# Performance work log

Hardware: AMD Instinct MI355X
Metric: run time of the kernel (lower is better)

The kernel has to match this reference:

```python
import jax, jax.numpy as jnp
import numpy as np

N_SV = 8192      # current-frame supervoxels (rows of mean_features / sv_prob)
M_SV = 8192      # surrounding-frame supervoxels
C_FEAT = 96
N_CLS = 20
EPSILON = 0.03   # OT entropic regularizer (forward default)


def setup_inputs() -> dict:
    key = jax.random.key(0)
    ks = jax.random.split(key, 8)
    # near-rigid poses: identity + small perturbation (keeps inverse well-conditioned)
    posses = jnp.eye(4, dtype=jnp.float32)[None] + 0.05 * jax.random.normal(ks[0], (2, 4, 4), jnp.float32)
    return {
        "sur_sv_feature": jax.random.normal(ks[1], (M_SV, C_FEAT), jnp.float32),
        "sur_sv_coords": jax.random.normal(ks[2], (M_SV, 3), jnp.float32),
        "sur_sv_gt": jax.random.randint(ks[3], (M_SV,), 0, N_CLS),
        "sv_prob": jax.random.normal(ks[4], (N_SV, N_CLS), jnp.float32),
        "mean_features": jax.random.normal(ks[5], (N_SV, C_FEAT), jnp.float32),
        "ori_coords": jax.random.normal(ks[6], (N_SV, 3), jnp.float32),
        "posses": posses,
        "sv_gt_idx": jax.random.randint(ks[7], (N_SV,), 0, N_SV),
        "lg": M_SV,
    }


def reference(sur_sv_feature, sur_sv_coords, sur_sv_gt, sv_prob, mean_features,
              ori_coords, posses, sv_gt_idx, lg):
    # --- alignment (rev=1 branch): transform surrounding coords into current frame ---
    diff = jnp.linalg.inv(posses[1]) @ posses[0]                      # [4,4]
    homo = jnp.concatenate([sur_sv_coords,
                            jnp.ones((sur_sv_coords.shape[0], 1), sur_sv_coords.dtype)], axis=1)
    al_sur = (homo @ diff.T)[:, :3]                                   # [M,3]

    # --- fused affinity construction: cosine + exp(-l2) kernel + support mask ---
    w1 = jnp.linalg.norm(mean_features, axis=1, keepdims=True)        # [N,1]
    w2 = jnp.linalg.norm(sur_sv_feature, axis=1, keepdims=True)      # [M,1]
    feat_dist = 1.0 - (mean_features @ sur_sv_feature.T) / jnp.clip(w1 * w2.T, 1e-8)  # [N,M]
    coords_dist = jnp.sum((ori_coords[:, None, :] - al_sur[None, :, :]) ** 2, -1) / (0.5 ** 2)  # [N,M]
    support = (coords_dist < 10.0 ** 2).astype(jnp.float32)
    dist_matric = 1.0 + feat_dist - jnp.exp(-0.5 * coords_dist)
    K = jnp.exp(-dist_matric / EPSILON) * support                     # [N,M]

    # --- Sinkhorn loop: original uses constant u1,u2 on the RHS, so a,b are
    # loop-invariant; a single evaluation reproduces all 10 iterations exactly ---
    N, M = K.shape
    u2 = jnp.full((N,), 1.0 / N, jnp.float32)
    u1 = jnp.full((M,), 1.0 / M, jnp.float32)
    b = u2 / (K @ u1 + 1e-16)                                         # [N]
    a = u1 / (K.T @ u2 + 1e-16)                                       # [M]

    simlarity = (a[:, None] * K.T) * b[None, :]                       # diag(a) @ K.T @ diag(b), [M,N]
    simlarity = simlarity[:lg]

    sv_prob_updated = jax.nn.softmax(sv_prob, axis=1)                 # [N,ncls]
    sm_index = jnp.argmax(simlarity, axis=1)                          # [lg] in [0,N)
    onehot = jax.nn.one_hot(sur_sv_gt, N_CLS, dtype=jnp.float32)      # [M,ncls]
    tmpx = jnp.argmax(onehot[:lg], axis=1)                            # [lg]
    conf = sv_prob_updated[sm_index, tmpx]                            # diag of gather
    tmp_hi = conf > 0.1
    tmp = jnp.where(jnp.any(tmp_hi), tmp_hi, conf > 0.0)              # fallback threshold

    # masked scatter: out-of-range index N drops the update (mode='drop')
    idx = jnp.where(tmp, sm_index, N)
    sv_prob_updated = sv_prob_updated.at[idx].set(onehot[:lg], mode="drop")
    trust = jnp.zeros((N,), bool).at[idx].set(True, mode="drop")      # fixed-shape unique(sm_index)
    pre = jnp.argmax(sv_prob_updated, axis=1)

    return trust, sv_prob_updated, pre, sm_index
```

## Files before the change

### kernel.cpp

```cpp
#include <hip/hip_runtime.h>
#include <math.h>

typedef __attribute__((ext_vector_type(8))) short short8;
typedef __attribute__((ext_vector_type(16))) float floatx16;

#define NSV 8192
#define MSV 8192
#define CF 96
#define NCLS 20

#define C48 48.08983469629878f
#define C96 96.17966939259756f
#define CEV -2.885390081777927f

#define OFF_A0    0u
#define OFF_A1    1572864u
#define OFF_A2    3145728u
#define OFF_B0    4718592u
#define OFF_B1    6291456u
#define OFF_B2    7864320u
#define OFF_RV4   9437184u
#define OFF_CV4   9568256u
#define OFF_PROW  9699328u
#define OFF_SMENC 11796480u
#define OFF_SMIDX 11862016u
#define OFF_WIN   11894784u
#define OFF_CONF  11927552u
#define OFF_FLAG  11960320u

#define O_TRUST 0
#define O_PROB  NSV
#define O_PRE   (O_PROB + NSV*NCLS)
#define O_SM    (O_PRE + NSV)

__device__ __forceinline__ unsigned short bfr(float x) {
  unsigned u = __float_as_uint(x);
  return (unsigned short)((u + 0x7FFFu + ((u >> 16) & 1u)) >> 16);
}
__device__ __forceinline__ float bff(unsigned short h) {
  return __uint_as_float(((unsigned)h) << 16);
}
__device__ __forceinline__ float fexp2(float x) {
  float r; asm("v_exp_f32 %0, %1" : "=v"(r) : "v"(x)); return r;
}

__global__ void k_prep(const float* __restrict__ surf, const float* __restrict__ surc,
                       const float* __restrict__ meanf, const float* __restrict__ ori,
                       const float* __restrict__ posses, char* __restrict__ wsb) {
  __shared__ float dsh[12];
  if (threadIdx.x == 0) {
    double m[4][8];
    for (int r = 0; r < 4; ++r)
      for (int c = 0; c < 4; ++c) { m[r][c] = (double)posses[16 + r*4 + c]; m[r][4+c] = (r == c) ? 1.0 : 0.0; }
    for (int col = 0; col < 4; ++col) {
      int piv = col; double best = fabs(m[col][col]);
      for (int r = col+1; r < 4; ++r) { double v = fabs(m[r][col]); if (v > best) { best = v; piv = r; } }
      if (piv != col) for (int c = 0; c < 8; ++c) { double tt = m[col][c]; m[col][c] = m[piv][c]; m[piv][c] = tt; }
      double pv = m[col][col];
      for (int c = 0; c < 8; ++c) m[col][c] /= pv;
      for (int r = 0; r < 4; ++r) if (r != col) {
        double f = m[r][col];
        for (int c = 0; c < 8; ++c) m[r][c] -= f * m[col][c];
      }
    }
    for (int r = 0; r < 3; ++r)
      for (int c = 0; c < 4; ++c) {
        double s = 0.0;
        for (int k = 0; k < 4; ++k) s += m[r][4+k] * (double)posses[k*4 + c];
        dsh[r*4 + c] = (float)s;
      }
  }
  __syncthreads();
  int j = blockIdx.x*256 + threadIdx.x;
  if (j >= NSV) return;
  float d[12];
  #pragma unroll
  for (int q = 0; q < 12; ++q) d[q] = dsh[q];
  float x = surc[j*3+0], y = surc[j*3+1], z = surc[j*3+2];
  float ax = ((x*d[0] + y*d[1]) + z*d[2]) + d[3];
  float ay = ((x*d[4] + y*d[5]) + z*d[6]) + d[7];
  float az = ((x*d[8] + y*d[9]) + z*d[10]) + d[11];
  const float4* f2 = (const float4*)(surf  + (size_t)j*CF);
  const float4* f1 = (const float4*)(meanf + (size_t)j*CF);
  float s2 = 0.f, s1 = 0.f;
  #pragma unroll
  for (int kq = 0; kq < 24; ++kq) {
    float4 v = f2[kq]; s2 += v.x*v.x; s2 += v.y*v.y; s2 += v.z*v.z; s2 += v.w*v.w;
  }
  #pragma unroll
  for (int kq = 0; kq < 24; ++kq) {
    float4 v = f1[kq]; s1 += v.x*v.x; s1 += v.y*v.y; s1 += v.z*v.z; s1 += v.w*v.w;
  }
  float4 cvv; cvv.x = 1.0f/sqrtf(s2); cvv.y = ax; cvv.z = ay; cvv.w = az;
  ((float4*)(wsb + OFF_CV4))[j] = cvv;
  float4 rvv; rvv.x = 1.0f/sqrtf(s1); rvv.y = ori[j*3+0]; rvv.z = ori[j*3+1]; rvv.w = ori[j*3+2];
  ((float4*)(wsb + OFF_RV4))[j] = rvv;
}

__global__ void k_split(const float* __restrict__ meanf, const float* __restrict__ surf,
                        char* __restrict__ wsb) {
  const int NT = NSV*CF/4;
  int idx = blockIdx.x*256 + threadIdx.x;
  if (idx >= 2*NT) return;
  int m = idx >= NT;
  int e4 = idx - (m ? NT : 0);
  int base4 = e4 * 4;
  int row = base4 / CF;
  int k0  = base4 - row*CF;
  const float* src = m ? surf : meanf;
  float scale;
  if (m) scale = ((const float4*)(wsb + OFF_CV4))[row].x;
  else   scale = ((const float4*)(wsb + OFF_RV4))[row].x * C48;
  unsigned short* d0 = (unsigned short*)(wsb + (m ? OFF_B0 : OFF_A0));
  unsigned short* d1 = (unsigned short*)(wsb + (m ? OFF_B1 : OFF_A1));
  unsigned short* d2 = (unsigned short*)(wsb + (m ? OFF_B2 : OFF_A2));
  float4 v = *(const float4*)(src + base4);
  float xs[4] = {v.x*scale, v.y*scale, v.z*scale, v.w*scale};
  unsigned short h0[4], h1[4], h2[4];
  #pragma unroll
  for (int c = 0; c < 4; ++c) {
    float x = xs[c];
    unsigned short a0 = bfr(x);  float r1 = x - bff(a0);
    unsigned short a1 = bfr(r1); float r2 = r1 - bff(a1);
    h0[c] = a0; h1[c] = a1; h2[c] = bfr(r2);
  }
  int g   = row >> 5;
  int l31 = row & 31;
  int kc  = k0 >> 4;
  int hi  = (k0 >> 3) & 1;
  int e8  = k0 & 7;
  int offu = ((g*6 + kc) << 9) + (((hi << 5) | l31) << 3) + e8;
  *(ushort4*)(d0 + offu) = make_ushort4(h0[0], h0[1], h0[2], h0[3]);
  *(ushort4*)(d1 + offu) = make_ushort4(h1[0], h1[1], h1[2], h1[3]);
  *(ushort4*)(d2 + offu) = make_ushort4(h2[0], h2[1], h2[2], h2[3]);
}

template<int PASS>
__global__ __launch_bounds__(256, 2)
void k_gemm(char* __restrict__ wsb) {
  const float4* RV  = (const float4*)(wsb + OFF_RV4);
  const float4* CVC = (const float4*)(wsb + OFF_CV4);
  float* PROW = (float*)(wsb + OFF_PROW);
  unsigned long long* SME = (unsigned long long*)(wsb + OFF_SMENC);

  __shared__ unsigned long long redbuf[2][128];

  int t = threadIdx.x, lane = t & 63, wid = t >> 6;
  int wr = wid >> 1, wc = wid & 1, l31 = lane & 31, hi = lane >> 5;
  int flat = blockIdx.y*64 + blockIdx.x;
  int xcd = flat & 7, q = flat >> 3;
  int xr = xcd >> 1, xc = xcd & 1;
  int bi = xr*16 + (q & 15), bj = xc*32 + (q >> 4);
  int I0 = bi*128, J0 = bj*128;

  const char* pA[3][2];
  const char* pB[3][2];
  {
    int gA = (I0 >> 5) + wr*2;
    int gB = (J0 >> 5) + wc*2;
    unsigned offs[3] = {OFF_A0, OFF_A1, OFF_A2};
    unsigned offsB[3] = {OFF_B0, OFF_B1, OFF_B2};
    #pragma unroll
    for (int s = 0; s < 3; ++s)
      #pragma unroll
      for (int ti = 0; ti < 2; ++ti) {
        pA[s][ti] = wsb + offs[s]  + (((gA + ti)*6) << 10) + lane*16;
        pB[s][ti] = wsb + offsB[s] + (((gB + ti)*6) << 10) + lane*16;
      }
  }

  floatx16 acc[2][2];
  #pragma unroll
  for (int ti = 0; ti < 2; ++ti)
    #pragma unroll
    for (int tj = 0; tj < 2; ++tj)
      #pragma unroll
      for (int e = 0; e < 16; ++e) acc[ti][tj][e] = 0.f;

  short8 fa[3][2], fb[3][2];
  #pragma unroll
  for (int s = 0; s < 3; ++s)
    #pragma unroll
    for (int ti = 0; ti < 2; ++ti) {
      fa[s][ti] = *(const short8*)(pA[s][ti]);
      fb[s][ti] = *(const short8*)(pB[s][ti]);
    }

  #pragma unroll
  for (int kc = 0; kc < 6; ++kc) {
    short8 na[3][2], nb[3][2];
    if (kc < 5) {
      #pragma unroll
      for (int s = 0; s < 3; ++s)
        #pragma unroll
        for (int ti = 0; ti < 2; ++ti) {
          na[s][ti] = *(const short8*)(pA[s][ti] + (kc+1)*1024);
          nb[s][ti] = *(const short8*)(pB[s][ti] + (kc+1)*1024);
        }
    }
    #pragma unroll
    for (int ti = 0; ti < 2; ++ti)
      #pragma unroll
      for (int tj = 0; tj < 2; ++tj) {
        acc[ti][tj] = __builtin_amdgcn_mfma_f32_32x32x16_bf16(fa[0][ti], fb[0][tj], acc[ti][tj], 0, 0, 0);
        acc[ti][tj] = __builtin_amdgcn_mfma_f32_32x32x16_bf16(fa[0][ti], fb[1][tj], acc[ti][tj], 0, 0, 0);
        acc[ti][tj] = __builtin_amdgcn_mfma_f32_32x32x16_bf16(fa[1][ti], fb[0][tj], acc[ti][tj], 0, 0, 0);
        acc[ti][tj] = __builtin_amdgcn_mfma_f32_32x32x16_bf16(fa[1][ti], fb[1][tj], acc[ti][tj], 0, 0, 0);
        acc[ti][tj] = __builtin_amdgcn_mfma_f32_32x32x16_bf16(fa[0][ti], fb[2][tj], acc[ti][tj], 0, 0, 0);
        acc[ti][tj] = __builtin_amdgcn_mfma_f32_32x32x16_bf16(fa[2][ti], fb[0][tj], acc[ti][tj], 0, 0, 0);
      }
    if (kc < 5) {
      #pragma unroll
      for (int s = 0; s < 3; ++s)
        #pragma unroll
        for (int ti = 0; ti < 2; ++ti) { fa[s][ti] = na[s][ti]; fb[s][ti] = nb[s][ti]; }
    }
  }

  float4 cv[2];
  #pragma unroll
  for (int tj = 0; tj < 2; ++tj) cv[tj] = CVC[J0 + wc*64 + tj*32 + l31];

  if (PASS == 1) {
    float* rowred = (float*)redbuf;
    #pragma unroll
    for (int ti = 0; ti < 2; ++ti) {
      #pragma unroll
      for (int r = 0; r < 16; ++r) {
        int lr = wr*64 + ti*32 + (r & 3) + 8*(r >> 2) + 4*hi;
        int row = I0 + lr;
        float4 rv = RV[row];
        float rowp = 0.f;
        #pragma unroll
        for (int tj = 0; tj < 2; ++tj) {
          float dotv = acc[ti][tj][r];
          float dx = rv.y - cv[tj].y, dy = rv.z - cv[tj].z, dz = rv.w - cv[tj].w;
          float s3 = fmaf(dz, dz, fmaf(dy, dy, dx*dx));
          float ev = fexp2(s3 * CEV);
          float kv = fexp2(fmaf(ev, C48, dotv - C96));
          kv = (s3 < 25.0f) ? kv : 0.0f;
          rowp += kv;
        }
        rowp += __shfl_xor(rowp, 1);
        rowp += __shfl_xor(rowp, 2);
        rowp += __shfl_xor(rowp, 4);
        rowp += __shfl_xor(rowp, 8);
        rowp += __shfl_xor(rowp, 16);
        if (l31 == 0) rowred[wc*128 + lr] = rowp;
      }
    }
    __syncthreads();
    if (t < 128) PROW[(size_t)(I0 + t)*64 + bj] = rowred[t] + rowred[128 + t];
  } else {
    unsigned long long benc[2] = {0ull, 0ull};
    #pragma unroll
    for (int ti = 0; ti < 2; ++ti) {
      #pragma unroll
      for (int r = 0; r < 16; ++r) {
        int lr = wr*64 + ti*32 + (r & 3) + 8*(r >> 2) + 4*hi;
        int row = I0 + lr;
        float4 rv = RV[row];
        unsigned rinv = 0xFFFFFFFFu - (unsigned)row;
        #pragma unroll
        for (int tj = 0; tj < 2; ++tj) {
          float dotv = acc[ti][tj][r];
          float dx = rv.y - cv[tj].y, dy = rv.z - cv[tj].z, dz = rv.w - cv[tj].w;
          float s3 = fmaf(dz, dz, fmaf(dy, dy, dx*dx));
          float ev = fexp2(s3 * CEV);
          float kv = fexp2(fmaf(ev, C48, dotv - C96));
          kv = (s3 < 25.0f) ? kv : 0.0f;
          float val = kv * rv.x;
          unsigned long long e = ((unsigned long long)__float_as_uint(val) << 32)
                               | (unsigned long long)rinv;
          benc[tj] = (e > benc[tj]) ? e : benc[tj];
        }
      }
    }
    #pragma unroll
    for (int tj = 0; tj < 2; ++tj) {
      unsigned long long o = __shfl_xor(benc[tj], 32);
      if (o > benc[tj]) benc[tj] = o;
      if (hi == 0) redbuf[wr][wc*64 + tj*32 + l31] = benc[tj];
    }
    __syncthreads();
    if (t < 128) {
      unsigned long long e0 = redbuf[0][t], e1 = redbuf[1][t];
      atomicMax(SME + (J0 + t), e0 > e1 ? e0 : e1);
    }
  }
}

__global__ void k_bvec(char* __restrict__ wsb) {
  int i = blockIdx.x*256 + threadIdx.x;
  if (i >= NSV) return;
  const float* p = (const float*)(wsb + OFF_PROW) + (size_t)i*64;
  float s = 0.f;
  #pragma unroll
  for (int q = 0; q < 64; ++q) s += p[q];
  float b = 0x1p-13f / (s * 0x1p-13f + 1e-16f);
  ((float*)(wsb + OFF_RV4))[(size_t)i*4] = b;
  ((int*)(wsb + OFF_WIN))[i] = -1;
  ((unsigned long long*)(wsb + OFF_SMENC))[i] = 0ull;
  if (i == 0) *((int*)(wsb + OFF_FLAG)) = 0;
}

__global__ void k_softmax(const float* __restrict__ svp, float* __restrict__ out) {
  int i = blockIdx.x*256 + threadIdx.x;
  if (i >= NSV) return;
  const float* x = svp + (size_t)i*NCLS;
  float mx = x[0];
  for (int c = 1; c < NCLS; ++c) mx = fmaxf(mx, x[c]);
  float e[NCLS]; float s = 0.f;
  for (int c = 0; c < NCLS; ++c) { e[c] = expf(x[c] - mx); s += e[c]; }
  float* p = out + O_PROB + (size_t)i*NCLS;
  for (int c = 0; c < NCLS; ++c) p[c] = e[c]/s;
}

__global__ void k_conf(const int* __restrict__ gt, char* __restrict__ wsb, float* __restrict__ out) {
  int j = blockIdx.x*256 + threadIdx.x;
  if (j >= MSV) return;
  unsigned long long enc = ((const unsigned long long*)(wsb + OFF_SMENC))[j];
  int sm = (int)(0xFFFFFFFFu - (unsigned)(enc & 0xFFFFFFFFull));
  ((int*)(wsb + OFF_SMIDX))[j] = sm;
  out[O_SM + j] = (float)sm;
  float c = out[O_PROB + (size_t)sm*NCLS + gt[j]];
  ((float*)(wsb + OFF_CONF))[j] = c;
  unsigned long long m = __ballot(c > 0.1f);
  if ((threadIdx.x & 63) == 0 && m) atomicOr((int*)(wsb + OFF_FLAG), 1);
}

__global__ void k_winner(char* __restrict__ wsb) {
  int j = blockIdx.x*256 + threadIdx.x;
  if (j >= MSV) return;
  float c = ((const float*)(wsb + OFF_CONF))[j];
  int f = *((const int*)(wsb + OFF_FLAG));
  bool tm = f ? (c > 0.1f) : (c > 0.0f);
  if (tm) atomicMax(((int*)(wsb + OFF_WIN)) + ((const int*)(wsb + OFF_SMIDX))[j], j);
}

__global__ void k_final(const int* __restrict__ gt, float* __restrict__ out, const char* __restrict__ wsb) {
  int i = blockIdx.x*256 + threadIdx.x;
  if (i >= NSV) return;
  int w = ((const int*)(wsb + OFF_WIN))[i];
  float* row = out + O_PROB + (size_t)i*NCLS;
  if (w >= 0) {
    int g = gt[w];
    for (int c = 0; c < NCLS; ++c) row[c] = (c == g) ? 1.f : 0.f;
  }
  out[O_TRUST + i] = (w >= 0) ? 1.f : 0.f;
  float mx = row[0]; int pi = 0;
  for (int c = 1; c < NCLS; ++c) { float v = row[c]; if (v > mx) { mx = v; pi = c; } }
  out[O_PRE + i] = (float)pi;
}

extern "C" void kernel_launch(void* const* d_in, const int* in_sizes, int n_in,
                              void* d_out, int out_size, void* d_ws, size_t ws_size,
                              hipStream_t stream) {
  const float* surf  = (const float*)d_in[0];
  const float* surc  = (const float*)d_in[1];
  const int*   gt    = (const int*)d_in[2];
  const float* svp   = (const float*)d_in[3];
  const float* meanf = (const float*)d_in[4];
  const float* ori   = (const float*)d_in[5];
  const float* poss  = (const float*)d_in[6];
  float* out = (float*)d_out;
  char* wsb = (char*)d_ws;

  k_prep<<<NSV/256, 256, 0, stream>>>(surf, surc, meanf, ori, poss, wsb);
  k_split<<<1536, 256, 0, stream>>>(meanf, surf, wsb);
  k_gemm<1><<<dim3(64, 64), 256, 0, stream>>>(wsb);
  k_bvec<<<NSV/256, 256, 0, stream>>>(wsb);
  k_gemm<2><<<dim3(64, 64), 256, 0, stream>>>(wsb);
  k_softmax<<<NSV/256, 256, 0, stream>>>(svp, out);
  k_conf<<<MSV/256, 256, 0, stream>>>(gt, wsb, out);
  k_winner<<<MSV/256, 256, 0, stream>>>(wsb);
  k_final<<<NSV/256, 256, 0, stream>>>(gt, out, wsb);
}
```

Before: 294.2 us.

## Stage GEMM operand tiles through LDS with direct global-to-LDS loads

Replaces per-wave direct global register loads of the bf16 split operands with cooperative global_load_lds staging of the block's A and B tiles into 72KB of shared memory, in two K-halves. Each wave then reads its fragments from LDS, so operand tiles shared by the waves of a block are fetched from global memory once rather than once per wave. In exchange the per-half loads are no longer overlapped with MFMA work, extra barriers are added, and the large LDS footprint may cut occupancy below the two blocks per CU that the launch bounds request.

```diff
diff --git a/kernel.cpp b/kernel.cpp
--- a/kernel.cpp
+++ b/kernel.cpp
@@ -143,6 +143,7 @@
   float* PROW = (float*)(wsb + OFF_PROW);
   unsigned long long* SME = (unsigned long long*)(wsb + OFF_SMENC);
 
+  __shared__ char lds[73728];
   __shared__ unsigned long long redbuf[2][128];
 
   int t = threadIdx.x, lane = t & 63, wid = t >> 6;
@@ -153,21 +154,27 @@
   int bi = xr*16 + (q & 15), bj = xc*32 + (q >> 4);
   int I0 = bi*128, J0 = bj*128;
 
-  const char* pA[3][2];
-  const char* pB[3][2];
-  {
-    int gA = (I0 >> 5) + wr*2;
-    int gB = (J0 >> 5) + wc*2;
-    unsigned offs[3] = {OFF_A0, OFF_A1, OFF_A2};
-    unsigned offsB[3] = {OFF_B0, OFF_B1, OFF_B2};
-    #pragma unroll
-    for (int s = 0; s < 3; ++s)
-      #pragma unroll
-      for (int ti = 0; ti < 2; ++ti) {
-        pA[s][ti] = wsb + offs[s]  + (((gA + ti)*6) << 10) + lane*16;
-        pB[s][ti] = wsb + offsB[s] + (((gB + ti)*6) << 10) + lane*16;
-      }
-  }
+  const unsigned offsA[3] = {OFF_A0, OFF_A1, OFF_A2};
+  const unsigned offsB[3] = {OFF_B0, OFF_B1, OFF_B2};
+
+  auto stage = [&](int h) {
+    #pragma unroll
+    for (int qq = 0; qq < 18; ++qq) {
+      int p = qq*4 + wid;
+      int side = (p >= 36) ? 1 : 0;
+      int r = p - side*36;
+      int s = r / 12;
+      int rem = r - s*12;
+      int gl = rem / 3;
+      int c = rem - gl*3;
+      unsigned base = side ? offsB[s] : offsA[s];
+      int g = ((side ? J0 : I0) >> 5) + gl;
+      const char* gp = wsb + base + (((unsigned)(g*6 + h*3 + c)) << 10) + lane*16;
+      char* lp = lds + p*1024 + lane*16;
+      __builtin_amdgcn_global_load_lds((const __attribute__((address_space(1))) void*)gp,
+                                       (__attribute__((address_space(3))) void*)lp, 16, 0, 0);
+    }
+  };
 
   floatx16 acc[2][2];
   #pragma unroll
@@ -177,45 +184,40 @@
       #pragma unroll
       for (int e = 0; e < 16; ++e) acc[ti][tj][e] = 0.f;
 
-  short8 fa[3][2], fb[3][2];
-  #pragma unroll
-  for (int s = 0; s < 3; ++s)
-    #pragma unroll
-    for (int ti = 0; ti < 2; ++ti) {
-      fa[s][ti] = *(const short8*)(pA[s][ti]);
-      fb[s][ti] = *(const short8*)(pB[s][ti]);
-    }
-
-  #pragma unroll
-  for (int kc = 0; kc < 6; ++kc) {
-    short8 na[3][2], nb[3][2];
-    if (kc < 5) {
+  auto compute_half = [&]() {
+    #pragma unroll
+    for (int c = 0; c < 3; ++c) {
+      short8 fa[3][2], fb[3][2];
       #pragma unroll
       for (int s = 0; s < 3; ++s)
         #pragma unroll
         for (int ti = 0; ti < 2; ++ti) {
-          na[s][ti] = *(const short8*)(pA[s][ti] + (kc+1)*1024);
-          nb[s][ti] = *(const short8*)(pB[s][ti] + (kc+1)*1024);
+          int pa = s*12 + (wr*2 + ti)*3 + c;
+          fa[s][ti] = *(const short8*)(lds + pa*1024 + lane*16);
+          int pb = 36 + s*12 + (wc*2 + ti)*3 + c;
+          fb[s][ti] = *(const short8*)(lds + pb*1024 + lane*16);
         }
-    }
-    #pragma unroll
-    for (int ti = 0; ti < 2; ++ti)
-      #pragma unroll
-      for (int tj = 0; tj < 2; ++tj) {
-        acc[ti][tj] = __builtin_amdgcn_mfma_f32_32x32x16_bf16(fa[0][ti], fb[0][tj], acc[ti][tj], 0, 0, 0);
-        acc[ti][tj] = __builtin_amdgcn_mfma_f32_32x32x16_bf16(fa[0][ti], fb[1][tj], acc[ti][tj], 0, 0, 0);
-        acc[ti][tj] = __builtin_amdgcn_mfma_f32_32x32x16_bf16(fa[1][ti], fb[0][tj], acc[ti][tj], 0, 0, 0);
-        acc[ti][tj] = __builtin_amdgcn_mfma_f32_32x32x16_bf16(fa[1][ti], fb[1][tj], acc[ti][tj], 0, 0, 0);
-        acc[ti][tj] = __builtin_amdgcn_mfma_f32_32x32x16_bf16(fa[0][ti], fb[2][tj], acc[ti][tj], 0, 0, 0);
-        acc[ti][tj] = __builtin_amdgcn_mfma_f32_32x32x16_bf16(fa[2][ti], fb[0][tj], acc[ti][tj], 0, 0, 0);
-      }
-    if (kc < 5) {
-      #pragma unroll
-      for (int s = 0; s < 3; ++s)
+      #pragma unroll
+      for (int ti = 0; ti < 2; ++ti)
         #pragma unroll
-        for (int ti = 0; ti < 2; ++ti) { fa[s][ti] = na[s][ti]; fb[s][ti] = nb[s][ti]; }
-    }
-  }
+        for (int tj = 0; tj < 2; ++tj) {
+          acc[ti][tj] = __builtin_amdgcn_mfma_f32_32x32x16_bf16(fa[0][ti], fb[0][tj], acc[ti][tj], 0, 0, 0);
+          acc[ti][tj] = __builtin_amdgcn_mfma_f32_32x32x16_bf16(fa[0][ti], fb[1][tj], acc[ti][tj], 0, 0, 0);
+          acc[ti][tj] = __builtin_amdgcn_mfma_f32_32x32x16_bf16(fa[1][ti], fb[0][tj], acc[ti][tj], 0, 0, 0);
+          acc[ti][tj] = __builtin_amdgcn_mfma_f32_32x32x16_bf16(fa[1][ti], fb[1][tj], acc[ti][tj], 0, 0, 0);
+          acc[ti][tj] = __builtin_amdgcn_mfma_f32_32x32x16_bf16(fa[0][ti], fb[2][tj], acc[ti][tj], 0, 0, 0);
+          acc[ti][tj] = __builtin_amdgcn_mfma_f32_32x32x16_bf16(fa[2][ti], fb[0][tj], acc[ti][tj], 0, 0, 0);
+        }
+    }
+  };
+
+  stage(0);
+  __syncthreads();
+  compute_half();
+  __syncthreads();
+  stage(1);
+  __syncthreads();
+  compute_half();
 
   float4 cv[2];
   #pragma unroll
```

After: 343.2 us. +16.7%, slower.
